# Performance work log

Measured on AMD Instinct MI355X. Metric: run time of the kernel, lower is better.

## Reference

```python
import jax, jax.numpy as jnp
import numpy as np

T, D, DL, E, I, SI = 2048, 2048, 1024, 64, 768, 4096
TOP_K, N_GROUP, TOPK_GROUP = 6, 8, 4
ROUTED_SCALE = 2.5
CAP = 384


def relu2(x):
    r = jnp.maximum(x, 0.0)
    return r * r


def setup_inputs() -> dict:
    key = jax.random.key(0)
    ks = jax.random.split(key, 9)
    return {
        "hidden_states": jax.random.normal(ks[0], (T, D), jnp.float32),
        "gate_w": jax.random.normal(ks[1], (E, D), jnp.float32) * 0.02,
        "gate_bias": jax.random.normal(ks[2], (E,), jnp.float32) * 0.01,  # e_score_correction_bias
        "fc1_w": jax.random.normal(ks[3], (DL, D), jnp.float32) * 0.02,
        "fc2_w": jax.random.normal(ks[4], (D, DL), jnp.float32) * 0.02,
        "w1": jax.random.normal(ks[5], (E, I, DL), jnp.float32) * 0.02,
        "w2": jax.random.normal(ks[6], (E, DL, I), jnp.float32) * 0.02,
        "sw1": jax.random.normal(ks[7], (SI, D), jnp.float32) * 0.02,
        "sw2": jax.random.normal(ks[8], (D, SI), jnp.float32) * 0.02,
    }


def reference(hidden_states, gate_w, gate_bias, fc1_w, fc2_w, w1, w2, sw1, sw2):
    x = hidden_states  # [T, D]
    # ---- DeepseekV3-style gate (sigmoid + bias-corrected group top-k) ----
    logits = x.astype(jnp.float32) @ gate_w.T.astype(jnp.float32)  # [T, E]
    scores = jax.nn.sigmoid(logits)
    sb = scores + gate_bias  # selection scores with correction bias
    gsb = sb.reshape(T, N_GROUP, E // N_GROUP)
    group_scores = jax.lax.top_k(gsb, 2)[0].sum(-1)  # [T, G] = sum of top-2 per group
    _, gidx = jax.lax.top_k(group_scores, TOPK_GROUP)
    gmask = jax.nn.one_hot(gidx, N_GROUP, dtype=sb.dtype).sum(1)  # [T, G]
    emask = jnp.repeat(gmask, E // N_GROUP, axis=1)  # [T, E]
    masked = jnp.where(emask > 0, sb, 0.0)
    _, tidx = jax.lax.top_k(masked, TOP_K)  # [T, K] selected expert ids
    tw = jnp.take_along_axis(scores, tidx, axis=1)  # weights from un-biased scores
    tw = tw / (tw.sum(-1, keepdims=True) + 1e-20) * ROUTED_SCALE  # [T, K]
    # ---- latent down-projection (fc1_latent_proj) ----
    xl = x @ fc1_w.T  # [T, DL]
    # ---- dispatch to per-expert buffers ----
    flat_e = tidx.reshape(-1)                 # [T*K]
    tok = jnp.repeat(jnp.arange(T), TOP_K)    # [T*K]
    oh = jax.nn.one_hot(flat_e, E, dtype=jnp.int32)              # [T*K, E]
    pos = jnp.sum((jnp.cumsum(oh, axis=0) - 1) * oh, axis=1)     # slot within expert
    valid = pos < CAP
    pos_c = jnp.where(valid, pos, 0)
    buf = jnp.zeros((E, CAP, DL), xl.dtype)
    buf = buf.at[flat_e, pos_c].add(jnp.where(valid[:, None], xl[tok], 0.0))
    # ---- grouped expert FFN: fc2(relu(fc1(x))^2) ----
    h = relu2(jnp.einsum('ecd,eid->eci', buf, w1))  # [E, CAP, I]
    out = jnp.einsum('eci,edi->ecd', h, w2)         # [E, CAP, DL]
    # ---- combine with routing weights ----
    gathered = out[flat_e, pos_c] * valid[:, None].astype(out.dtype)  # [T*K, DL]
    routed = jnp.sum(gathered.reshape(T, TOP_K, DL) * tw[..., None].astype(out.dtype), axis=1)
    routed = routed @ fc2_w.T  # fc2_latent_proj, [T, D]
    # ---- shared experts (relu2 MLP) run in parallel ----
    shared = relu2(x @ sw1.T) @ sw2.T  # [T, D]
    return shared + routed
```

## Files before the change

kernel.cpp:

```cpp
#include <hip/hip_runtime.h>

typedef unsigned int u32;
typedef unsigned short u16;
typedef __attribute__((ext_vector_type(4))) float floatx4;
typedef __attribute__((ext_vector_type(8))) __bf16 bf16x8;

#define T_ 2048
#define D_ 2048
#define DL_ 1024
#define E_ 64
#define I_ 768
#define SI_ 4096
#define TOPK 6
#define NGRP 8
#define TOPG 4
#define CAP_ 384

#define BM 128
#define BN 128
#define BK 32

__device__ __forceinline__ u16 f2bf(float f) {
  u32 u = __builtin_bit_cast(u32, f);
  u += 0x7fffu + ((u >> 16) & 1u);
  return (u16)(u >> 16);
}
__device__ __forceinline__ float bf2f(u16 h) {
  return __builtin_bit_cast(float, ((u32)h) << 16);
}

__device__ __forceinline__ void async16(const u16* g, u16* l) {
  __builtin_amdgcn_global_load_lds((const __attribute__((address_space(1))) void*)g,
                                   (__attribute__((address_space(3))) void*)l, 16, 0, 0);
}

__global__ __launch_bounds__(256) void cvt_f2b_k(const float* __restrict__ src,
                                                 u16* __restrict__ dst, int n8) {
  int i = blockIdx.x * 256 + threadIdx.x;
  if (i >= n8) return;
  const float4* s4 = (const float4*)src;
  float4 a = s4[2 * i], b = s4[2 * i + 1];
  u32 p0 = (u32)f2bf(a.x) | ((u32)f2bf(a.y) << 16);
  u32 p1 = (u32)f2bf(a.z) | ((u32)f2bf(a.w) << 16);
  u32 p2 = (u32)f2bf(b.x) | ((u32)f2bf(b.y) << 16);
  u32 p3 = (u32)f2bf(b.z) | ((u32)f2bf(b.w) << 16);
  ((uint4*)dst)[i] = make_uint4(p0, p1, p2, p3);
}

__global__ __launch_bounds__(256) void gate_logits_k(const float* __restrict__ x,
                                                     const float* __restrict__ gw,
                                                     float* __restrict__ logits) {
  __shared__ float xs[16 * 65];
  __shared__ float wsd[64 * 65];
  const int tid = threadIdx.x;
  const int t0 = blockIdx.x * 16;
  const int tl = tid & 15, eb = (tid >> 4) * 4;
  const int xr = tid >> 4, xc = (tid & 15) * 4;
  const int wr = tid >> 2, wc = (tid & 3) * 16;
  float acc[4] = {0.f, 0.f, 0.f, 0.f};
  for (int kc = 0; kc < D_; kc += 64) {
    __syncthreads();
    float4 xv = *(const float4*)&x[(size_t)(t0 + xr) * D_ + kc + xc];
    xs[xr * 65 + xc + 0] = xv.x;
    xs[xr * 65 + xc + 1] = xv.y;
    xs[xr * 65 + xc + 2] = xv.z;
    xs[xr * 65 + xc + 3] = xv.w;
#pragma unroll
    for (int i = 0; i < 4; ++i) {
      float4 wv = *(const float4*)&gw[(size_t)wr * D_ + kc + wc + i * 4];
      wsd[wr * 65 + wc + i * 4 + 0] = wv.x;
      wsd[wr * 65 + wc + i * 4 + 1] = wv.y;
      wsd[wr * 65 + wc + i * 4 + 2] = wv.z;
      wsd[wr * 65 + wc + i * 4 + 3] = wv.w;
    }
    __syncthreads();
#pragma unroll 4
    for (int kk = 0; kk < 64; ++kk) {
      float xvv = xs[tl * 65 + kk];
#pragma unroll
      for (int q = 0; q < 4; ++q) acc[q] += xvv * wsd[(eb + q) * 65 + kk];
    }
  }
#pragma unroll
  for (int q = 0; q < 4; ++q) logits[(size_t)(t0 + tl) * E_ + eb + q] = acc[q];
}

__global__ __launch_bounds__(256) void route_k(const float* __restrict__ logits,
                                               const float* __restrict__ bias,
                                               int* __restrict__ cnts,
                                               int* __restrict__ etok,
                                               int* __restrict__ row_of,
                                               float* __restrict__ tww) {
  int t = blockIdx.x * 256 + threadIdx.x;
  if (t >= T_) return;
  float s[E_], cand[E_];
  float gs[NGRP];
  for (int e = 0; e < E_; ++e) {
    float lg = logits[(size_t)t * E_ + e];
    float sv = 1.f / (1.f + __expf(-lg));
    s[e] = sv;
    cand[e] = sv + bias[e];
  }
  for (int g = 0; g < NGRP; ++g) {
    float m1 = -1e30f, m2 = -1e30f;
    for (int j = 0; j < 8; ++j) {
      float v = cand[g * 8 + j];
      if (v > m1) { m2 = m1; m1 = v; }
      else if (v > m2) m2 = v;
    }
    gs[g] = m1 + m2;
  }
  bool gsel[NGRP];
  for (int g = 0; g < NGRP; ++g) gsel[g] = false;
  for (int r = 0; r < TOPG; ++r) {
    float best = -1e30f; int bi = 0;
    for (int g = 0; g < NGRP; ++g)
      if (!gsel[g] && gs[g] > best) { best = gs[g]; bi = g; }
    gsel[bi] = true;
  }
  for (int e = 0; e < E_; ++e)
    if (!gsel[e >> 3]) cand[e] = 0.0f;
  float wsum = 0.f; int eid[TOPK]; float wv[TOPK];
  for (int r = 0; r < TOPK; ++r) {
    float best = -1e30f; int bi = 0;
    for (int e = 0; e < E_; ++e)
      if (cand[e] > best) { best = cand[e]; bi = e; }
    cand[bi] = -1e30f;
    eid[r] = bi; wv[r] = s[bi]; wsum += s[bi];
  }
  float inv = 2.5f / (wsum + 1e-20f);
  for (int r = 0; r < TOPK; ++r) {
    int e = eid[r];
    int slot = atomicAdd(&cnts[e], 1);
    int rowid = -1;
    if (slot < CAP_) { rowid = e * CAP_ + slot; etok[rowid] = t; }
    row_of[t * TOPK + r] = rowid;
    tww[t * TOPK + r] = wv[r] * inv;
  }
}

template <int EPI, bool GATHER>
__global__ __launch_bounds__(256) void gemm_bf(const u16* __restrict__ A,
                                               const u16* __restrict__ B,
                                               void* __restrict__ Cp,
                                               int M, int K, int ldA, int ldB, int ldC,
                                               long sAe, long sBe, long sCe,
                                               const int* __restrict__ counts,
                                               const int* __restrict__ gather) {
  __shared__ u16 As[BM * BK];
  __shared__ u16 Bs[BN * BK];
  const int e = blockIdx.z;
  int Mloc = M;
  if (counts) { Mloc = counts[e]; if (Mloc > CAP_) Mloc = CAP_; }
  const int m0 = blockIdx.y * BM;
  if (m0 >= Mloc) return;
  const int n0 = blockIdx.x * BN;
  const int tid = threadIdx.x;
  const int wave = tid >> 6, lane = tid & 63;
  const int lrow = lane >> 2;
  const int lcol = (lane & 3) * 8;

  int ar0 = m0 + wave * 32 + lrow;
  int ar1 = ar0 + 16;
  const u16 *aS0, *aS1;
  if (GATHER) {
    int t0i = (ar0 < Mloc) ? gather[e * CAP_ + ar0] : 0;
    int t1i = (ar1 < Mloc) ? gather[e * CAP_ + ar1] : 0;
    aS0 = A + (size_t)t0i * ldA + lcol;
    aS1 = A + (size_t)t1i * ldA + lcol;
  } else {
    aS0 = A + (size_t)e * sAe + (size_t)ar0 * ldA + lcol;
    aS1 = A + (size_t)e * sAe + (size_t)ar1 * ldA + lcol;
  }
  int br0 = n0 + wave * 32 + lrow, br1 = br0 + 16;
  const u16* bS0 = B + (size_t)e * sBe + (size_t)br0 * ldB + lcol;
  const u16* bS1 = B + (size_t)e * sBe + (size_t)br1 * ldB + lcol;

  u16* lA0 = &As[(wave * 32 + 0) * BK];
  u16* lA1 = &As[(wave * 32 + 16) * BK];
  u16* lB0 = &Bs[(wave * 32 + 0) * BK];
  u16* lB1 = &Bs[(wave * 32 + 16) * BK];

  floatx4 acc[4][4];
#pragma unroll
  for (int i = 0; i < 4; ++i)
#pragma unroll
    for (int j = 0; j < 4; ++j) acc[i][j] = floatx4{0.f, 0.f, 0.f, 0.f};

  const int wm = (wave & 1) * 64, wn = (wave >> 1) * 64;
  const int lr = lane & 15, lk = (lane >> 4) * 8;

  for (int kt = 0; kt < K; kt += BK) {
    __syncthreads();
    async16(aS0 + kt, lA0);
    async16(aS1 + kt, lA1);
    async16(bS0 + kt, lB0);
    async16(bS1 + kt, lB1);
    __syncthreads();
    bf16x8 af[4], bfr[4];
#pragma unroll
    for (int i = 0; i < 4; ++i)
      af[i] = *(const bf16x8*)&As[(wm + i * 16 + lr) * BK + lk];
#pragma unroll
    for (int j = 0; j < 4; ++j)
      bfr[j] = *(const bf16x8*)&Bs[(wn + j * 16 + lr) * BK + lk];
#pragma unroll
    for (int i = 0; i < 4; ++i)
#pragma unroll
      for (int j = 0; j < 4; ++j)
        acc[i][j] = __builtin_amdgcn_mfma_f32_16x16x32_bf16(af[i], bfr[j], acc[i][j], 0, 0, 0);
  }

  const int rbase = (lane >> 4) * 4;
#pragma unroll
  for (int i = 0; i < 4; ++i) {
#pragma unroll
    for (int r = 0; r < 4; ++r) {
      int grow = m0 + wm + i * 16 + rbase + r;
      if (grow >= Mloc) continue;
      size_t crow = (size_t)sCe * e + (size_t)grow * ldC;
#pragma unroll
      for (int j = 0; j < 4; ++j) {
        int gcol = n0 + wn + j * 16 + lr;
        float v = acc[i][j][r];
        if constexpr (EPI == 0) {
          ((u16*)Cp)[crow + gcol] = f2bf(v);
        } else if constexpr (EPI == 1) {
          v = fmaxf(v, 0.f); v *= v;
          ((u16*)Cp)[crow + gcol] = f2bf(v);
        } else if constexpr (EPI == 2) {
          ((float*)Cp)[crow + gcol] = v;
        } else {
          ((float*)Cp)[crow + gcol] += v;
        }
      }
    }
  }
}

#define LDS_PAD 40
template <int ATYPE, int EPI>
__global__ __launch_bounds__(256, 2) void gemm_nt(const void* __restrict__ Ap,
                                                  const float* __restrict__ Bp,
                                                  void* __restrict__ Cp,
                                                  int M, int K, int ldA, int ldB, int ldC,
                                                  long sAe, long sBe, long sCe,
                                                  const int* __restrict__ counts,
                                                  const int* __restrict__ gather) {
  __shared__ u16 As[BM * LDS_PAD];
  __shared__ u16 Bs[BN * LDS_PAD];
  const int e = blockIdx.z;
  int Mloc = M;
  if (counts) { Mloc = counts[e]; if (Mloc > CAP_) Mloc = CAP_; }
  const int m0 = blockIdx.y * BM;
  if (m0 >= Mloc) return;
  const int n0 = blockIdx.x * BN;
  const int tid = threadIdx.x;
  const int row = tid >> 1;
  const int colb = (tid & 1) * 16;
  const int arow = m0 + row;
  int arowIdx;
  if (gather) arowIdx = (arow < Mloc) ? gather[e * CAP_ + arow] : 0;
  else arowIdx = arow;
  const float* Af32 = (const float*)Ap + (size_t)e * sAe + (size_t)arowIdx * ldA;
  const u16* Abf = (const u16*)Ap + (size_t)e * sAe + (size_t)arowIdx * ldA;
  const float* Brow = Bp + (size_t)e * sBe + (size_t)(n0 + row) * ldB;
  float4 ra[4]; uint4 rab[2]; float4 rb[4];
  auto loadAB = [&](int kt) {
    if constexpr (ATYPE == 0) {
#pragma unroll
      for (int i = 0; i < 4; ++i) ra[i] = *(const float4*)&Af32[kt + colb + i * 4];
    } else {
#pragma unroll
      for (int i = 0; i < 2; ++i) rab[i] = *(const uint4*)&Abf[kt + colb + i * 8];
    }
#pragma unroll
    for (int i = 0; i < 4; ++i) rb[i] = *(const float4*)&Brow[kt + colb + i * 4];
  };
  auto stage = [&]() {
    uint4* ad = (uint4*)&As[row * LDS_PAD + colb];
    if constexpr (ATYPE == 0) {
      u32 w[8];
#pragma unroll
      for (int i = 0; i < 4; ++i) {
        w[2 * i] = (u32)f2bf(ra[i].x) | ((u32)f2bf(ra[i].y) << 16);
        w[2 * i + 1] = (u32)f2bf(ra[i].z) | ((u32)f2bf(ra[i].w) << 16);
      }
      ad[0] = make_uint4(w[0], w[1], w[2], w[3]);
      ad[1] = make_uint4(w[4], w[5], w[6], w[7]);
    } else {
      ad[0] = rab[0]; ad[1] = rab[1];
    }
    u32 wb[8];
#pragma unroll
    for (int i = 0; i < 4; ++i) {
      wb[2 * i] = (u32)f2bf(rb[i].x) | ((u32)f2bf(rb[i].y) << 16);
      wb[2 * i + 1] = (u32)f2bf(rb[i].z) | ((u32)f2bf(rb[i].w) << 16);
    }
    uint4* bd = (uint4*)&Bs[row * LDS_PAD + colb];
    bd[0] = make_uint4(wb[0], wb[1], wb[2], wb[3]);
    bd[1] = make_uint4(wb[4], wb[5], wb[6], wb[7]);
  };
  floatx4 acc[4][4];
#pragma unroll
  for (int i = 0; i < 4; ++i)
#pragma unroll
    for (int j = 0; j < 4; ++j) acc[i][j] = floatx4{0.f, 0.f, 0.f, 0.f};
  const int wave = tid >> 6, lane = tid & 63;
  const int wm = (wave & 1) * 64, wn = (wave >> 1) * 64;
  const int lr = lane & 15, lk = (lane >> 4) * 8;
  loadAB(0);
  for (int kt = 0; kt < K; kt += BK) {
    __syncthreads();
    stage();
    __syncthreads();
    if (kt + BK < K) loadAB(kt + BK);
    bf16x8 af[4], bfr[4];
#pragma unroll
    for (int i = 0; i < 4; ++i)
      af[i] = *(const bf16x8*)&As[(wm + i * 16 + lr) * LDS_PAD + lk];
#pragma unroll
    for (int j = 0; j < 4; ++j)
      bfr[j] = *(const bf16x8*)&Bs[(wn + j * 16 + lr) * LDS_PAD + lk];
#pragma unroll
    for (int i = 0; i < 4; ++i)
#pragma unroll
      for (int j = 0; j < 4; ++j)
        acc[i][j] = __builtin_amdgcn_mfma_f32_16x16x32_bf16(af[i], bfr[j], acc[i][j], 0, 0, 0);
  }
  const int rbase = (lane >> 4) * 4;
#pragma unroll
  for (int i = 0; i < 4; ++i) {
#pragma unroll
    for (int r = 0; r < 4; ++r) {
      int grow = m0 + wm + i * 16 + rbase + r;
      if (grow >= Mloc) continue;
      size_t crow = (size_t)sCe * e + (size_t)grow * ldC;
#pragma unroll
      for (int j = 0; j < 4; ++j) {
        int gcol = n0 + wn + j * 16 + lr;
        float v = acc[i][j][r];
        if constexpr (EPI == 0) {
          ((u16*)Cp)[crow + gcol] = f2bf(v);
        } else if constexpr (EPI == 1) {
          v = fmaxf(v, 0.f); v *= v;
          ((u16*)Cp)[crow + gcol] = f2bf(v);
        } else if constexpr (EPI == 2) {
          ((float*)Cp)[crow + gcol] = v;
        } else {
          ((float*)Cp)[crow + gcol] += v;
        }
      }
    }
  }
}

__global__ __launch_bounds__(256) void combine_k(const u16* __restrict__ eout,
                                                 const int* __restrict__ row_of,
                                                 const float* __restrict__ tww,
                                                 u16* __restrict__ ylat) {
  int t = blockIdx.x;
  int c0 = threadIdx.x * 4;
  float a0 = 0.f, a1 = 0.f, a2 = 0.f, a3 = 0.f;
#pragma unroll
  for (int k = 0; k < TOPK; ++k) {
    int r = row_of[t * TOPK + k];
    float w = tww[t * TOPK + k];
    if (r >= 0) {
      uint2 v = *(const uint2*)&eout[(size_t)r * DL_ + c0];
      a0 += w * bf2f((u16)(v.x & 0xffffu));
      a1 += w * bf2f((u16)(v.x >> 16));
      a2 += w * bf2f((u16)(v.y & 0xffffu));
      a3 += w * bf2f((u16)(v.y >> 16));
    }
  }
  u32 o0 = (u32)f2bf(a0) | ((u32)f2bf(a1) << 16);
  u32 o1 = (u32)f2bf(a2) | ((u32)f2bf(a3) << 16);
  *(uint2*)&ylat[(size_t)t * DL_ + c0] = make_uint2(o0, o1);
}

extern "C" void kernel_launch(void* const* d_in, const int* in_sizes, int n_in,
                              void* d_out, int out_size, void* d_ws, size_t ws_size,
                              hipStream_t stream) {
  (void)in_sizes; (void)n_in; (void)out_size;
  const float* x = (const float*)d_in[0];
  const float* gw = (const float*)d_in[1];
  const float* gbias = (const float*)d_in[2];
  const float* fc1 = (const float*)d_in[3];
  const float* fc2 = (const float*)d_in[4];
  const float* w1 = (const float*)d_in[5];
  const float* w2 = (const float*)d_in[6];
  const float* sw1 = (const float*)d_in[7];
  const float* sw2 = (const float*)d_in[8];
  float* out = (float*)d_out;

  char* ws = (char*)d_ws;
  size_t off = 0;
  auto alloc = [&](size_t bytes) {
    char* p = ws + off;
    off += (bytes + 255) & ~(size_t)255;
    return p;
  };
  float* logits = (float*)alloc((size_t)T_ * E_ * 4);
  int* cnts = (int*)alloc(E_ * 4);
  int* etok = (int*)alloc((size_t)E_ * CAP_ * 4);
  int* row_of = (int*)alloc((size_t)T_ * TOPK * 4);
  float* tww = (float*)alloc((size_t)T_ * TOPK * 4);
  u16* xl = (u16*)alloc((size_t)T_ * DL_ * 2);
  u16* ylat = (u16*)alloc((size_t)T_ * DL_ * 2);

  size_t big1_elems = (size_t)E_ * CAP_ * I_;
  if ((size_t)T_ * SI_ > big1_elems) big1_elems = (size_t)T_ * SI_;
  size_t need_fast = off + (((size_t)T_ * D_ * 2 + 255) & ~255ul)
                     + (((size_t)D_ * DL_ * 2 + 255) & ~255ul)
                     + ((big1_elems * 2 + 255) & ~255ul)
                     + (((size_t)E_ * CAP_ * DL_ * 2 + 255) & ~255ul)
                     + (((size_t)E_ * I_ * DL_ * 2 + 255) & ~255ul);

  hipMemsetAsync(cnts, 0, E_ * 4, stream);
  gate_logits_k<<<T_ / 16, 256, 0, stream>>>(x, gw, logits);
  route_k<<<T_ / 256, 256, 0, stream>>>(logits, gbias, cnts, etok, row_of, tww);

  if (ws_size >= need_fast) {
    u16* xbf = (u16*)alloc((size_t)T_ * D_ * 2);
    u16* fc2b = (u16*)alloc((size_t)D_ * DL_ * 2);
    u16* big1 = (u16*)alloc(big1_elems * 2);
    u16* eoutB = (u16*)alloc((size_t)E_ * CAP_ * DL_ * 2);
    u16* wbuf = (u16*)alloc((size_t)E_ * I_ * DL_ * 2);
    u16* sw1b = wbuf;
    u16* sw2b = wbuf + (size_t)SI_ * D_;
    u16* fc1b = wbuf + 2 * (size_t)SI_ * D_;

    cvt_f2b_k<<<(T_ * D_ / 8 + 255) / 256, 256, 0, stream>>>(x, xbf, T_ * D_ / 8);
    cvt_f2b_k<<<(SI_ * D_ / 8 + 255) / 256, 256, 0, stream>>>(sw1, sw1b, SI_ * D_ / 8);
    cvt_f2b_k<<<(SI_ * D_ / 8 + 255) / 256, 256, 0, stream>>>(sw2, sw2b, SI_ * D_ / 8);
    cvt_f2b_k<<<(DL_ * D_ / 8 + 255) / 256, 256, 0, stream>>>(fc1, fc1b, DL_ * D_ / 8);
    cvt_f2b_k<<<(D_ * DL_ / 8 + 255) / 256, 256, 0, stream>>>(fc2, fc2b, D_ * DL_ / 8);

    gemm_bf<1, false><<<dim3(SI_ / BN, T_ / BM, 1), 256, 0, stream>>>(
        xbf, sw1b, big1, T_, D_, D_, D_, SI_, 0, 0, 0, nullptr, nullptr);
    gemm_bf<2, false><<<dim3(D_ / BN, T_ / BM, 1), 256, 0, stream>>>(
        big1, sw2b, out, T_, SI_, SI_, SI_, D_, 0, 0, 0, nullptr, nullptr);

    gemm_bf<0, false><<<dim3(DL_ / BN, T_ / BM, 1), 256, 0, stream>>>(
        xbf, fc1b, xl, T_, D_, D_, D_, DL_, 0, 0, 0, nullptr, nullptr);

    int nw = E_ * I_ * DL_ / 8;
    cvt_f2b_k<<<(nw + 255) / 256, 256, 0, stream>>>(w1, wbuf, nw);
    gemm_bf<1, true><<<dim3(I_ / BN, CAP_ / BM, E_), 256, 0, stream>>>(
        xl, wbuf, big1, CAP_, DL_, DL_, DL_, I_,
        0, (long)I_ * DL_, (long)CAP_ * I_, cnts, etok);

    cvt_f2b_k<<<(nw + 255) / 256, 256, 0, stream>>>(w2, wbuf, nw);
    gemm_bf<0, false><<<dim3(DL_ / BN, CAP_ / BM, E_), 256, 0, stream>>>(
        big1, wbuf, eoutB, CAP_, I_, I_, I_, DL_,
        (long)CAP_ * I_, (long)DL_ * I_, (long)CAP_ * DL_, cnts, nullptr);

    combine_k<<<T_, 256, 0, stream>>>(eoutB, row_of, tww, ylat);

    gemm_bf<3, false><<<dim3(D_ / BN, T_ / BM, 1), 256, 0, stream>>>(
        ylat, fc2b, out, T_, DL_, DL_, DL_, D_, 0, 0, 0, nullptr, nullptr);
  } else {
    char* big = alloc((size_t)E_ * CAP_ * I_ * 2 + (size_t)E_ * CAP_ * DL_ * 2);
    u16* hs = (u16*)big;
    u16* h = (u16*)big;
    u16* eoutB = (u16*)(big + (size_t)E_ * CAP_ * I_ * 2);

    gemm_nt<0, 1><<<dim3(SI_ / BN, T_ / BM, 1), 256, 0, stream>>>(
        x, sw1, hs, T_, D_, D_, D_, SI_, 0, 0, 0, nullptr, nullptr);
    gemm_nt<1, 2><<<dim3(D_ / BN, T_ / BM, 1), 256, 0, stream>>>(
        hs, sw2, out, T_, SI_, SI_, SI_, D_, 0, 0, 0, nullptr, nullptr);
    gemm_nt<0, 0><<<dim3(DL_ / BN, T_ / BM, 1), 256, 0, stream>>>(
        x, fc1, xl, T_, D_, D_, D_, DL_, 0, 0, 0, nullptr, nullptr);
    gemm_nt<1, 1><<<dim3(I_ / BN, CAP_ / BM, E_), 256, 0, stream>>>(
        xl, w1, h, CAP_, DL_, DL_, DL_, I_,
        0, (long)I_ * DL_, (long)CAP_ * I_, cnts, etok);
    gemm_nt<1, 0><<<dim3(DL_ / BN, CAP_ / BM, E_), 256, 0, stream>>>(
        h, w2, eoutB, CAP_, I_, I_, I_, DL_,
        (long)CAP_ * I_, (long)DL_ * I_, (long)CAP_ * DL_, cnts, nullptr);
    combine_k<<<T_, 256, 0, stream>>>(eoutB, row_of, tww, ylat);
    gemm_nt<1, 3><<<dim3(D_ / BN, T_ / BM, 1), 256, 0, stream>>>(
        ylat, fc2, out, T_, DL_, DL_, DL_, D_, 0, 0, 0, nullptr, nullptr);
  }
}
```

Before: 979.3 us.

## Double-buffer bf16 GEMM, add narrow-N tiles, parallelize gate and routing

The bf16 GEMM now double-buffers its LDS tiles so the async global-to-LDS load for the next K step is issued before the current step's MFMAs run. It also gains a BNT template parameter, and the shared down-projection, fc1 and fc2 GEMMs use 64-wide N tiles to launch more blocks. The gate logits kernel is split across two expert halves for more parallelism, and routing is rewritten so one wavefront handles one token using shuffle and ballot reductions instead of serial per-thread loops. In exchange, LDS use per block doubles, and the narrow tiles do less reuse per load.

```diff
diff --git a/kernel.cpp b/kernel.cpp
--- a/kernel.cpp
+++ b/kernel.cpp
@@ -17,7 +17,6 @@
 #define CAP_ 384
 
 #define BM 128
-#define BN 128
 #define BK 32
 
 __device__ __forceinline__ u16 f2bf(float f) {
@@ -51,13 +50,14 @@
                                                      const float* __restrict__ gw,
                                                      float* __restrict__ logits) {
   __shared__ float xs[16 * 65];
-  __shared__ float wsd[64 * 65];
+  __shared__ float wsd[32 * 65];
   const int tid = threadIdx.x;
   const int t0 = blockIdx.x * 16;
-  const int tl = tid & 15, eb = (tid >> 4) * 4;
+  const int e0 = blockIdx.y * 32;
+  const int tl = tid & 15, eb = (tid >> 4) * 2;
   const int xr = tid >> 4, xc = (tid & 15) * 4;
-  const int wr = tid >> 2, wc = (tid & 3) * 16;
-  float acc[4] = {0.f, 0.f, 0.f, 0.f};
+  const int wr = tid >> 3, wc = (tid & 7) * 8;
+  float acc[2] = {0.f, 0.f};
   for (int kc = 0; kc < D_; kc += 64) {
     __syncthreads();
     float4 xv = *(const float4*)&x[(size_t)(t0 + xr) * D_ + kc + xc];
@@ -66,8 +66,8 @@
     xs[xr * 65 + xc + 2] = xv.z;
     xs[xr * 65 + xc + 3] = xv.w;
 #pragma unroll
-    for (int i = 0; i < 4; ++i) {
-      float4 wv = *(const float4*)&gw[(size_t)wr * D_ + kc + wc + i * 4];
+    for (int i = 0; i < 2; ++i) {
+      float4 wv = *(const float4*)&gw[(size_t)(e0 + wr) * D_ + kc + wc + i * 4];
       wsd[wr * 65 + wc + i * 4 + 0] = wv.x;
       wsd[wr * 65 + wc + i * 4 + 1] = wv.y;
       wsd[wr * 65 + wc + i * 4 + 2] = wv.z;
@@ -77,12 +77,12 @@
 #pragma unroll 4
     for (int kk = 0; kk < 64; ++kk) {
       float xvv = xs[tl * 65 + kk];
-#pragma unroll
-      for (int q = 0; q < 4; ++q) acc[q] += xvv * wsd[(eb + q) * 65 + kk];
-    }
-  }
-#pragma unroll
-  for (int q = 0; q < 4; ++q) logits[(size_t)(t0 + tl) * E_ + eb + q] = acc[q];
+      acc[0] += xvv * wsd[eb * 65 + kk];
+      acc[1] += xvv * wsd[(eb + 1) * 65 + kk];
+    }
+  }
+  logits[(size_t)(t0 + tl) * E_ + e0 + eb + 0] = acc[0];
+  logits[(size_t)(t0 + tl) * E_ + e0 + eb + 1] = acc[1];
 }
 
 __global__ __launch_bounds__(256) void route_k(const float* __restrict__ logits,
@@ -91,55 +91,63 @@
                                                int* __restrict__ etok,
                                                int* __restrict__ row_of,
                                                float* __restrict__ tww) {
-  int t = blockIdx.x * 256 + threadIdx.x;
-  if (t >= T_) return;
-  float s[E_], cand[E_];
-  float gs[NGRP];
-  for (int e = 0; e < E_; ++e) {
-    float lg = logits[(size_t)t * E_ + e];
-    float sv = 1.f / (1.f + __expf(-lg));
-    s[e] = sv;
-    cand[e] = sv + bias[e];
-  }
-  for (int g = 0; g < NGRP; ++g) {
-    float m1 = -1e30f, m2 = -1e30f;
-    for (int j = 0; j < 8; ++j) {
-      float v = cand[g * 8 + j];
-      if (v > m1) { m2 = m1; m1 = v; }
-      else if (v > m2) m2 = v;
-    }
-    gs[g] = m1 + m2;
-  }
-  bool gsel[NGRP];
-  for (int g = 0; g < NGRP; ++g) gsel[g] = false;
+  const int wid = threadIdx.x >> 6, lane = threadIdx.x & 63;
+  const int t = blockIdx.x * 4 + wid;
+  float lg = logits[(size_t)t * E_ + lane];
+  float s = 1.f / (1.f + __expf(-lg));
+  float sb = s + bias[lane];
+  const int g = lane >> 3;
+  float m1 = sb;
+  m1 = fmaxf(m1, __shfl_xor(m1, 1));
+  m1 = fmaxf(m1, __shfl_xor(m1, 2));
+  m1 = fmaxf(m1, __shfl_xor(m1, 4));
+  unsigned long long b1 = __ballot(sb == m1);
+  int am = __ffsll((unsigned long long)((b1 >> (g * 8)) & 0xFFull)) - 1 + g * 8;
+  float v2 = (lane == am) ? -1e30f : sb;
+  float m2 = v2;
+  m2 = fmaxf(m2, __shfl_xor(m2, 1));
+  m2 = fmaxf(m2, __shfl_xor(m2, 2));
+  m2 = fmaxf(m2, __shfl_xor(m2, 4));
+  float gs = m1 + m2;
+  float gsv[NGRP];
+#pragma unroll
+  for (int gg = 0; gg < NGRP; ++gg) gsv[gg] = __shfl(gs, gg * 8);
+  unsigned selm = 0;
+#pragma unroll
   for (int r = 0; r < TOPG; ++r) {
     float best = -1e30f; int bi = 0;
-    for (int g = 0; g < NGRP; ++g)
-      if (!gsel[g] && gs[g] > best) { best = gs[g]; bi = g; }
-    gsel[bi] = true;
-  }
-  for (int e = 0; e < E_; ++e)
-    if (!gsel[e >> 3]) cand[e] = 0.0f;
-  float wsum = 0.f; int eid[TOPK]; float wv[TOPK];
+#pragma unroll
+    for (int gg = 0; gg < NGRP; ++gg)
+      if (!((selm >> gg) & 1) && gsv[gg] > best) { best = gsv[gg]; bi = gg; }
+    selm |= 1u << bi;
+  }
+  float val = ((selm >> g) & 1) ? sb : 0.0f;
+  float wsum = 0.f; int selr = -1;
+#pragma unroll
   for (int r = 0; r < TOPK; ++r) {
-    float best = -1e30f; int bi = 0;
-    for (int e = 0; e < E_; ++e)
-      if (cand[e] > best) { best = cand[e]; bi = e; }
-    cand[bi] = -1e30f;
-    eid[r] = bi; wv[r] = s[bi]; wsum += s[bi];
+    float m = val;
+    m = fmaxf(m, __shfl_xor(m, 1));
+    m = fmaxf(m, __shfl_xor(m, 2));
+    m = fmaxf(m, __shfl_xor(m, 4));
+    m = fmaxf(m, __shfl_xor(m, 8));
+    m = fmaxf(m, __shfl_xor(m, 16));
+    m = fmaxf(m, __shfl_xor(m, 32));
+    unsigned long long b2 = __ballot(val == m);
+    int am2 = __ffsll(b2) - 1;
+    if (lane == am2) { selr = r; val = -1e30f; }
+    wsum += __shfl(s, am2);
   }
   float inv = 2.5f / (wsum + 1e-20f);
-  for (int r = 0; r < TOPK; ++r) {
-    int e = eid[r];
-    int slot = atomicAdd(&cnts[e], 1);
+  if (selr >= 0) {
+    int slot = atomicAdd(&cnts[lane], 1);
     int rowid = -1;
-    if (slot < CAP_) { rowid = e * CAP_ + slot; etok[rowid] = t; }
-    row_of[t * TOPK + r] = rowid;
-    tww[t * TOPK + r] = wv[r] * inv;
-  }
-}
-
-template <int EPI, bool GATHER>
+    if (slot < CAP_) { rowid = lane * CAP_ + slot; etok[rowid] = t; }
+    row_of[t * TOPK + selr] = rowid;
+    tww[t * TOPK + selr] = s * inv;
+  }
+}
+
+template <int EPI, bool GATHER, int BNT>
 __global__ __launch_bounds__(256) void gemm_bf(const u16* __restrict__ A,
                                                const u16* __restrict__ B,
                                                void* __restrict__ Cp,
@@ -147,14 +155,15 @@
                                                long sAe, long sBe, long sCe,
                                                const int* __restrict__ counts,
                                                const int* __restrict__ gather) {
-  __shared__ u16 As[BM * BK];
-  __shared__ u16 Bs[BN * BK];
+  constexpr int NJ = BNT / 32;
+  __shared__ u16 As[2][BM * BK];
+  __shared__ u16 Bs[2][BNT * BK];
   const int e = blockIdx.z;
   int Mloc = M;
   if (counts) { Mloc = counts[e]; if (Mloc > CAP_) Mloc = CAP_; }
   const int m0 = blockIdx.y * BM;
   if (m0 >= Mloc) return;
-  const int n0 = blockIdx.x * BN;
+  const int n0 = blockIdx.x * BNT;
   const int tid = threadIdx.x;
   const int wave = tid >> 6, lane = tid & 63;
   const int lrow = lane >> 2;
@@ -162,7 +171,7 @@
 
   int ar0 = m0 + wave * 32 + lrow;
   int ar1 = ar0 + 16;
-  const u16 *aS0, *aS1;
+  const u16 *aS0, *aS1, *bS0, *bS1 = nullptr;
   if (GATHER) {
     int t0i = (ar0 < Mloc) ? gather[e * CAP_ + ar0] : 0;
     int t1i = (ar1 < Mloc) ? gather[e * CAP_ + ar1] : 0;
@@ -172,45 +181,173 @@
     aS0 = A + (size_t)e * sAe + (size_t)ar0 * ldA + lcol;
     aS1 = A + (size_t)e * sAe + (size_t)ar1 * ldA + lcol;
   }
-  int br0 = n0 + wave * 32 + lrow, br1 = br0 + 16;
-  const u16* bS0 = B + (size_t)e * sBe + (size_t)br0 * ldB + lcol;
-  const u16* bS1 = B + (size_t)e * sBe + (size_t)br1 * ldB + lcol;
-
-  u16* lA0 = &As[(wave * 32 + 0) * BK];
-  u16* lA1 = &As[(wave * 32 + 16) * BK];
-  u16* lB0 = &Bs[(wave * 32 + 0) * BK];
-  u16* lB1 = &Bs[(wave * 32 + 16) * BK];
-
+  if (BNT == 128) {
+    int br0 = n0 + wave * 32 + lrow;
+    bS0 = B + (size_t)e * sBe + (size_t)br0 * ldB + lcol;
+    bS1 = B + (size_t)e * sBe + (size_t)(br0 + 16) * ldB + lcol;
+  } else {
+    int br0 = n0 + wave * 16 + lrow;
+    bS0 = B + (size_t)e * sBe + (size_t)br0 * ldB + lcol;
+  }
+
+  auto issue = [&](int kt, int p) {
+    async16(aS0 + kt, &As[p][(wave * 32 + 0) * BK]);
+    async16(aS1 + kt, &As[p][(wave * 32 + 16) * BK]);
+    if (BNT == 128) {
+      async16(bS0 + kt, &Bs[p][(wave * 32 + 0) * BK]);
+      async16(bS1 + kt, &Bs[p][(wave * 32 + 16) * BK]);
+    } else {
+      async16(bS0 + kt, &Bs[p][(wave * 16) * BK]);
+    }
+  };
+
+  floatx4 acc[4][NJ];
+#pragma unroll
+  for (int i = 0; i < 4; ++i)
+#pragma unroll
+    for (int j = 0; j < NJ; ++j) acc[i][j] = floatx4{0.f, 0.f, 0.f, 0.f};
+
+  const int wm = (wave & 1) * 64;
+  const int wn = (wave >> 1) * (BNT == 128 ? 64 : 32);
+  const int lr = lane & 15, lk = (lane >> 4) * 8;
+
+  issue(0, 0);
+  int p = 0;
+  for (int kt = 0; kt < K; kt += BK, p ^= 1) {
+    __syncthreads();
+    if (kt + BK < K) issue(kt + BK, p ^ 1);
+    bf16x8 af[4], bfr[NJ];
+#pragma unroll
+    for (int i = 0; i < 4; ++i)
+      af[i] = *(const bf16x8*)&As[p][(wm + i * 16 + lr) * BK + lk];
+#pragma unroll
+    for (int j = 0; j < NJ; ++j)
+      bfr[j] = *(const bf16x8*)&Bs[p][(wn + j * 16 + lr) * BK + lk];
+#pragma unroll
+    for (int i = 0; i < 4; ++i)
+#pragma unroll
+      for (int j = 0; j < NJ; ++j)
+        acc[i][j] = __builtin_amdgcn_mfma_f32_16x16x32_bf16(af[i], bfr[j], acc[i][j], 0, 0, 0);
+  }
+
+  const int rbase = (lane >> 4) * 4;
+#pragma unroll
+  for (int i = 0; i < 4; ++i) {
+#pragma unroll
+    for (int r = 0; r < 4; ++r) {
+      int grow = m0 + wm + i * 16 + rbase + r;
+      if (grow >= Mloc) continue;
+      size_t crow = (size_t)sCe * e + (size_t)grow * ldC;
+#pragma unroll
+      for (int j = 0; j < NJ; ++j) {
+        int gcol = n0 + wn + j * 16 + lr;
+        float v = acc[i][j][r];
+        if constexpr (EPI == 0) {
+          ((u16*)Cp)[crow + gcol] = f2bf(v);
+        } else if constexpr (EPI == 1) {
+          v = fmaxf(v, 0.f); v *= v;
+          ((u16*)Cp)[crow + gcol] = f2bf(v);
+        } else if constexpr (EPI == 2) {
+          ((float*)Cp)[crow + gcol] = v;
+        } else {
+          ((float*)Cp)[crow + gcol] += v;
+        }
+      }
+    }
+  }
+}
+
+#define LDS_PAD 40
+#define BNF 128
+template <int ATYPE, int EPI>
+__global__ __launch_bounds__(256, 2) void gemm_nt(const void* __restrict__ Ap,
+                                                  const float* __restrict__ Bp,
+                                                  void* __restrict__ Cp,
+                                                  int M, int K, int ldA, int ldB, int ldC,
+                                                  long sAe, long sBe, long sCe,
+                                                  const int* __restrict__ counts,
+                                                  const int* __restrict__ gather) {
+  __shared__ u16 As[BM * LDS_PAD];
+  __shared__ u16 Bs[BNF * LDS_PAD];
+  const int e = blockIdx.z;
+  int Mloc = M;
+  if (counts) { Mloc = counts[e]; if (Mloc > CAP_) Mloc = CAP_; }
+  const int m0 = blockIdx.y * BM;
+  if (m0 >= Mloc) return;
+  const int n0 = blockIdx.x * BNF;
+  const int tid = threadIdx.x;
+  const int row = tid >> 1;
+  const int colb = (tid & 1) * 16;
+  const int arow = m0 + row;
+  int arowIdx;
+  if (gather) arowIdx = (arow < Mloc) ? gather[e * CAP_ + arow] : 0;
+  else arowIdx = arow;
+  const float* Af32 = (const float*)Ap + (size_t)e * sAe + (size_t)arowIdx * ldA;
+  const u16* Abf = (const u16*)Ap + (size_t)e * sAe + (size_t)arowIdx * ldA;
+  const float* Brow = Bp + (size_t)e * sBe + (size_t)(n0 + row) * ldB;
+  float4 ra[4]; uint4 rab[2]; float4 rb[4];
+  auto loadAB = [&](int kt) {
+    if constexpr (ATYPE == 0) {
+#pragma unroll
+      for (int i = 0; i < 4; ++i) ra[i] = *(const float4*)&Af32[kt + colb + i * 4];
+    } else {
+#pragma unroll
+      for (int i = 0; i < 2; ++i) rab[i] = *(const uint4*)&Abf[kt + colb + i * 8];
+    }
+#pragma unroll
+    for (int i = 0; i < 4; ++i) rb[i] = *(const float4*)&Brow[kt + colb + i * 4];
+  };
+  auto stage = [&]() {
+    uint4* ad = (uint4*)&As[row * LDS_PAD + colb];
+    if constexpr (ATYPE == 0) {
+      u32 w[8];
+#pragma unroll
+      for (int i = 0; i < 4; ++i) {
+        w[2 * i] = (u32)f2bf(ra[i].x) | ((u32)f2bf(ra[i].y) << 16);
+        w[2 * i + 1] = (u32)f2bf(ra[i].z) | ((u32)f2bf(ra[i].w) << 16);
+      }
+      ad[0] = make_uint4(w[0], w[1], w[2], w[3]);
+      ad[1] = make_uint4(w[4], w[5], w[6], w[7]);
+    } else {
+      ad[0] = rab[0]; ad[1] = rab[1];
+    }
+    u32 wb[8];
+#pragma unroll
+    for (int i = 0; i < 4; ++i) {
+      wb[2 * i] = (u32)f2bf(rb[i].x) | ((u32)f2bf(rb[i].y) << 16);
+      wb[2 * i + 1] = (u32)f2bf(rb[i].z) | ((u32)f2bf(rb[i].w) << 16);
+    }
+    uint4* bd = (uint4*)&Bs[row * LDS_PAD + colb];
+    bd[0] = make_uint4(wb[0], wb[1], wb[2], wb[3]);
+    bd[1] = make_uint4(wb[4], wb[5], wb[6], wb[7]);
+  };
   floatx4 acc[4][4];
 #pragma unroll
   for (int i = 0; i < 4; ++i)
 #pragma unroll
     for (int j = 0; j < 4; ++j) acc[i][j] = floatx4{0.f, 0.f, 0.f, 0.f};
-
+  const int wave = tid >> 6, lane = tid & 63;
   const int wm = (wave & 1) * 64, wn = (wave >> 1) * 64;
   const int lr = lane & 15, lk = (lane >> 4) * 8;
-
+  loadAB(0);
   for (int kt = 0; kt < K; kt += BK) {
     __syncthreads();
-    async16(aS0 + kt, lA0);
-    async16(aS1 + kt, lA1);
-    async16(bS0 + kt, lB0);
-    async16(bS1 + kt, lB1);
+    stage();
     __syncthreads();
+    if (kt + BK < K) loadAB(kt + BK);
     bf16x8 af[4], bfr[4];
 #pragma unroll
     for (int i = 0; i < 4; ++i)
-      af[i] = *(const bf16x8*)&As[(wm + i * 16 + lr) * BK + lk];
+      af[i] = *(const bf16x8*)&As[(wm + i * 16 + lr) * LDS_PAD + lk];
 #pragma unroll
     for (int j = 0; j < 4; ++j)
-      bfr[j] = *(const bf16x8*)&Bs[(wn + j * 16 + lr) * BK + lk];
+      bfr[j] = *(const bf16x8*)&Bs[(wn + j * 16 + lr) * LDS_PAD + lk];
 #pragma unroll
     for (int i = 0; i < 4; ++i)
 #pragma unroll
       for (int j = 0; j < 4; ++j)
         acc[i][j] = __builtin_amdgcn_mfma_f32_16x16x32_bf16(af[i], bfr[j], acc[i][j], 0, 0, 0);
   }
-
   const int rbase = (lane >> 4) * 4;
 #pragma unroll
   for (int i = 0; i < 4; ++i) {
@@ -238,123 +375,6 @@
   }
 }
 
-#define LDS_PAD 40
-template <int ATYPE, int EPI>
-__global__ __launch_bounds__(256, 2) void gemm_nt(const void* __restrict__ Ap,
-                                                  const float* __restrict__ Bp,
-                                                  void* __restrict__ Cp,
-                                                  int M, int K, int ldA, int ldB, int ldC,
-                                                  long sAe, long sBe, long sCe,
-                                                  const int* __restrict__ counts,
-                                                  const int* __restrict__ gather) {
-  __shared__ u16 As[BM * LDS_PAD];
-  __shared__ u16 Bs[BN * LDS_PAD];
-  const int e = blockIdx.z;
-  int Mloc = M;
-  if (counts) { Mloc = counts[e]; if (Mloc > CAP_) Mloc = CAP_; }
-  const int m0 = blockIdx.y * BM;
-  if (m0 >= Mloc) return;
-  const int n0 = blockIdx.x * BN;
-  const int tid = threadIdx.x;
-  const int row = tid >> 1;
-  const int colb = (tid & 1) * 16;
-  const int arow = m0 + row;
-  int arowIdx;
-  if (gather) arowIdx = (arow < Mloc) ? gather[e * CAP_ + arow] : 0;
-  else arowIdx = arow;
-  const float* Af32 = (const float*)Ap + (size_t)e * sAe + (size_t)arowIdx * ldA;
-  const u16* Abf = (const u16*)Ap + (size_t)e * sAe + (size_t)arowIdx * ldA;
-  const float* Brow = Bp + (size_t)e * sBe + (size_t)(n0 + row) * ldB;
-  float4 ra[4]; uint4 rab[2]; float4 rb[4];
-  auto loadAB = [&](int kt) {
-    if constexpr (ATYPE == 0) {
-#pragma unroll
-      for (int i = 0; i < 4; ++i) ra[i] = *(const float4*)&Af32[kt + colb + i * 4];
-    } else {
-#pragma unroll
-      for (int i = 0; i < 2; ++i) rab[i] = *(const uint4*)&Abf[kt + colb + i * 8];
-    }
-#pragma unroll
-    for (int i = 0; i < 4; ++i) rb[i] = *(const float4*)&Brow[kt + colb + i * 4];
-  };
-  auto stage = [&]() {
-    uint4* ad = (uint4*)&As[row * LDS_PAD + colb];
-    if constexpr (ATYPE == 0) {
-      u32 w[8];
-#pragma unroll
-      for (int i = 0; i < 4; ++i) {
-        w[2 * i] = (u32)f2bf(ra[i].x) | ((u32)f2bf(ra[i].y) << 16);
-        w[2 * i + 1] = (u32)f2bf(ra[i].z) | ((u32)f2bf(ra[i].w) << 16);
-      }
-      ad[0] = make_uint4(w[0], w[1], w[2], w[3]);
-      ad[1] = make_uint4(w[4], w[5], w[6], w[7]);
-    } else {
-      ad[0] = rab[0]; ad[1] = rab[1];
-    }
-    u32 wb[8];
-#pragma unroll
-    for (int i = 0; i < 4; ++i) {
-      wb[2 * i] = (u32)f2bf(rb[i].x) | ((u32)f2bf(rb[i].y) << 16);
-      wb[2 * i + 1] = (u32)f2bf(rb[i].z) | ((u32)f2bf(rb[i].w) << 16);
-    }
-    uint4* bd = (uint4*)&Bs[row * LDS_PAD + colb];
-    bd[0] = make_uint4(wb[0], wb[1], wb[2], wb[3]);
-    bd[1] = make_uint4(wb[4], wb[5], wb[6], wb[7]);
-  };
-  floatx4 acc[4][4];
-#pragma unroll
-  for (int i = 0; i < 4; ++i)
-#pragma unroll
-    for (int j = 0; j < 4; ++j) acc[i][j] = floatx4{0.f, 0.f, 0.f, 0.f};
-  const int wave = tid >> 6, lane = tid & 63;
-  const int wm = (wave & 1) * 64, wn = (wave >> 1) * 64;
-  const int lr = lane & 15, lk = (lane >> 4) * 8;
-  loadAB(0);
-  for (int kt = 0; kt < K; kt += BK) {
-    __syncthreads();
-    stage();
-    __syncthreads();
-    if (kt + BK < K) loadAB(kt + BK);
-    bf16x8 af[4], bfr[4];
-#pragma unroll
-    for (int i = 0; i < 4; ++i)
-      af[i] = *(const bf16x8*)&As[(wm + i * 16 + lr) * LDS_PAD + lk];
-#pragma unroll
-    for (int j = 0; j < 4; ++j)
-      bfr[j] = *(const bf16x8*)&Bs[(wn + j * 16 + lr) * LDS_PAD + lk];
-#pragma unroll
-    for (int i = 0; i < 4; ++i)
-#pragma unroll
-      for (int j = 0; j < 4; ++j)
-        acc[i][j] = __builtin_amdgcn_mfma_f32_16x16x32_bf16(af[i], bfr[j], acc[i][j], 0, 0, 0);
-  }
-  const int rbase = (lane >> 4) * 4;
-#pragma unroll
-  for (int i = 0; i < 4; ++i) {
-#pragma unroll
-    for (int r = 0; r < 4; ++r) {
-      int grow = m0 + wm + i * 16 + rbase + r;
-      if (grow >= Mloc) continue;
-      size_t crow = (size_t)sCe * e + (size_t)grow * ldC;
-#pragma unroll
-      for (int j = 0; j < 4; ++j) {
-        int gcol = n0 + wn + j * 16 + lr;
-        float v = acc[i][j][r];
-        if constexpr (EPI == 0) {
-          ((u16*)Cp)[crow + gcol] = f2bf(v);
-        } else if constexpr (EPI == 1) {
-          v = fmaxf(v, 0.f); v *= v;
-          ((u16*)Cp)[crow + gcol] = f2bf(v);
-        } else if constexpr (EPI == 2) {
-          ((float*)Cp)[crow + gcol] = v;
-        } else {
-          ((float*)Cp)[crow + gcol] += v;
-        }
-      }
-    }
-  }
-}
-
 __global__ __launch_bounds__(256) void combine_k(const u16* __restrict__ eout,
                                                  const int* __restrict__ row_of,
                                                  const float* __restrict__ tww,
@@ -418,8 +438,8 @@
                      + (((size_t)E_ * I_ * DL_ * 2 + 255) & ~255ul);
 
   hipMemsetAsync(cnts, 0, E_ * 4, stream);
-  gate_logits_k<<<T_ / 16, 256, 0, stream>>>(x, gw, logits);
-  route_k<<<T_ / 256, 256, 0, stream>>>(logits, gbias, cnts, etok, row_of, tww);
+  gate_logits_k<<<dim3(T_ / 16, 2), 256, 0, stream>>>(x, gw, logits);
+  route_k<<<T_ / 4, 256, 0, stream>>>(logits, gbias, cnts, etok, row_of, tww);
 
   if (ws_size >= need_fast) {
     u16* xbf = (u16*)alloc((size_t)T_ * D_ * 2);
@@ -437,28 +457,28 @@
     cvt_f2b_k<<<(DL_ * D_ / 8 + 255) / 256, 256, 0, stream>>>(fc1, fc1b, DL_ * D_ / 8);
     cvt_f2b_k<<<(D_ * DL_ / 8 + 255) / 256, 256, 0, stream>>>(fc2, fc2b, D_ * DL_ / 8);
 
-    gemm_bf<1, false><<<dim3(SI_ / BN, T_ / BM, 1), 256, 0, stream>>>(
+    gemm_bf<1, false, 128><<<dim3(SI_ / 128, T_ / BM, 1), 256, 0, stream>>>(
         xbf, sw1b, big1, T_, D_, D_, D_, SI_, 0, 0, 0, nullptr, nullptr);
-    gemm_bf<2, false><<<dim3(D_ / BN, T_ / BM, 1), 256, 0, stream>>>(
+    gemm_bf<2, false, 64><<<dim3(D_ / 64, T_ / BM, 1), 256, 0, stream>>>(
         big1, sw2b, out, T_, SI_, SI_, SI_, D_, 0, 0, 0, nullptr, nullptr);
 
-    gemm_bf<0, false><<<dim3(DL_ / BN, T_ / BM, 1), 256, 0, stream>>>(
+    gemm_bf<0, false, 64><<<dim3(DL_ / 64, T_ / BM, 1), 256, 0, stream>>>(
         xbf, fc1b, xl, T_, D_, D_, D_, DL_, 0, 0, 0, nullptr, nullptr);
 
     int nw = E_ * I_ * DL_ / 8;
     cvt_f2b_k<<<(nw + 255) / 256, 256, 0, stream>>>(w1, wbuf, nw);
-    gemm_bf<1, true><<<dim3(I_ / BN, CAP_ / BM, E_), 256, 0, stream>>>(
+    gemm_bf<1, true, 128><<<dim3(I_ / 128, CAP_ / BM, E_), 256, 0, stream>>>(
         xl, wbuf, big1, CAP_, DL_, DL_, DL_, I_,
         0, (long)I_ * DL_, (long)CAP_ * I_, cnts, etok);
 
     cvt_f2b_k<<<(nw + 255) / 256, 256, 0, stream>>>(w2, wbuf, nw);
-    gemm_bf<0, false><<<dim3(DL_ / BN, CAP_ / BM, E_), 256, 0, stream>>>(
+    gemm_bf<0, false, 128><<<dim3(DL_ / 128, CAP_ / BM, E_), 256, 0, stream>>>(
         big1, wbuf, eoutB, CAP_, I_, I_, I_, DL_,
         (long)CAP_ * I_, (long)DL_ * I_, (long)CAP_ * DL_, cnts, nullptr);
 
     combine_k<<<T_, 256, 0, stream>>>(eoutB, row_of, tww, ylat);
 
-    gemm_bf<3, false><<<dim3(D_ / BN, T_ / BM, 1), 256, 0, stream>>>(
+    gemm_bf<3, false, 64><<<dim3(D_ / 64, T_ / BM, 1), 256, 0, stream>>>(
         ylat, fc2b, out, T_, DL_, DL_, DL_, D_, 0, 0, 0, nullptr, nullptr);
   } else {
     char* big = alloc((size_t)E_ * CAP_ * I_ * 2 + (size_t)E_ * CAP_ * DL_ * 2);
@@ -466,20 +486,20 @@
     u16* h = (u16*)big;
     u16* eoutB = (u16*)(big + (size_t)E_ * CAP_ * I_ * 2);
 
-    gemm_nt<0, 1><<<dim3(SI_ / BN, T_ / BM, 1), 256, 0, stream>>>(
+    gemm_nt<0, 1><<<dim3(SI_ / BNF, T_ / BM, 1), 256, 0, stream>>>(
         x, sw1, hs, T_, D_, D_, D_, SI_, 0, 0, 0, nullptr, nullptr);
-    gemm_nt<1, 2><<<dim3(D_ / BN, T_ / BM, 1), 256, 0, stream>>>(
+    gemm_nt<1, 2><<<dim3(D_ / BNF, T_ / BM, 1), 256, 0, stream>>>(
         hs, sw2, out, T_, SI_, SI_, SI_, D_, 0, 0, 0, nullptr, nullptr);
-    gemm_nt<0, 0><<<dim3(DL_ / BN, T_ / BM, 1), 256, 0, stream>>>(
+    gemm_nt<0, 0><<<dim3(DL_ / BNF, T_ / BM, 1), 256, 0, stream>>>(
         x, fc1, xl, T_, D_, D_, D_, DL_, 0, 0, 0, nullptr, nullptr);
-    gemm_nt<1, 1><<<dim3(I_ / BN, CAP_ / BM, E_), 256, 0, stream>>>(
+    gemm_nt<1, 1><<<dim3(I_ / BNF, CAP_ / BM, E_), 256, 0, stream>>>(
         xl, w1, h, CAP_, DL_, DL_, DL_, I_,
         0, (long)I_ * DL_, (long)CAP_ * I_, cnts, etok);
-    gemm_nt<1, 0><<<dim3(DL_ / BN, CAP_ / BM, E_), 256, 0, stream>>>(
+    gemm_nt<1, 0><<<dim3(DL_ / BNF, CAP_ / BM, E_), 256, 0, stream>>>(
         h, w2, eoutB, CAP_, I_, I_, I_, DL_,
         (long)CAP_ * I_, (long)DL_ * I_, (long)CAP_ * DL_, cnts, nullptr);
     combine_k<<<T_, 256, 0, stream>>>(eoutB, row_of, tww, ylat);
-    gemm_nt<1, 3><<<dim3(D_ / BN, T_ / BM, 1), 256, 0, stream>>>(
+    gemm_nt<1, 3><<<dim3(D_ / BNF, T_ / BM, 1), 256, 0, stream>>>(
         ylat, fc2, out, T_, DL_, DL_, DL_, D_, 0, 0, 0, nullptr, nullptr);
   }
 }
```

Measured after the change: 884.1 us. -9.7%, faster.
